# Kernel optimization log

Hardware: AMD Instinct MI355X
Metric: run time of the kernel (lower is better)

## Reference

```python
import jax, jax.numpy as jnp
import numpy as np

NUM_TREES = 150
ARITY = 4
DEPTH = 4
NUM_LEVELS = DEPTH + 1  # leaves (level 0) ... root (level DEPTH)
VOCAB = 10000
SUBTOK = 8
EMB_DIM = 256
HID = 256
NUM_CLASSES = 2


def _build_forest():
    # perfect ARITY-ary tree, level-order indexing; edges point child -> parent
    n = (ARITY ** (DEPTH + 1) - 1) // (ARITY - 1)  # 341
    src = np.arange(1, n)
    dst = (src - 1) // ARITY
    depth_of = np.zeros(n, dtype=np.int64)
    for j in range(1, n):
        depth_of[j] = depth_of[(j - 1) // ARITY] + 1
    level_of = DEPTH - depth_of  # leaves = 0, processed first (topo order)
    offs = np.arange(NUM_TREES) * n
    edge_src = (src[None, :] + offs[:, None]).ravel().astype(np.int32)
    edge_dst = (dst[None, :] + offs[:, None]).ravel().astype(np.int32)
    node_level = np.tile(level_of, NUM_TREES).astype(np.int32)
    graph_id = np.repeat(np.arange(NUM_TREES), n).astype(np.int32)
    leaf_mask = (node_level == 0).astype(np.int32)
    return edge_src, edge_dst, node_level, graph_id, leaf_mask, NUM_TREES * n


def setup_inputs() -> dict:
    key = jax.random.key(0)
    ks = jax.random.split(key, 16)
    es, ed, lvl, gid, lm, N = _build_forest()
    s_e = 1.0 / np.sqrt(EMB_DIM)
    s_h = 1.0 / np.sqrt(HID)
    s_f = 1.0 / np.sqrt(2 * HID)
    return {
        "node_feat1": jax.random.randint(ks[0], (N, SUBTOK), 0, VOCAB, dtype=jnp.int32),
        "node_feat2": jax.random.randint(ks[1], (N, SUBTOK), 0, VOCAB, dtype=jnp.int32),
        "emb1": jax.random.normal(ks[2], (VOCAB, EMB_DIM), jnp.float32) * 0.02,
        "emb2": jax.random.normal(ks[3], (VOCAB, EMB_DIM), jnp.float32) * 0.02,
        "W_iou1": jax.random.normal(ks[4], (EMB_DIM, 3 * HID), jnp.float32) * s_e,
        "W_iou2": jax.random.normal(ks[5], (EMB_DIM, 3 * HID), jnp.float32) * s_e,
        "U_iou1": jax.random.normal(ks[6], (HID, 3 * HID), jnp.float32) * s_h,
        "U_iou2": jax.random.normal(ks[7], (HID, 3 * HID), jnp.float32) * s_h,
        "Uf_W1": jax.random.normal(ks[8], (HID, HID), jnp.float32) * s_h,
        "Uf_b1": jnp.zeros((HID,), jnp.float32),
        "Uf_W2": jax.random.normal(ks[9], (HID, HID), jnp.float32) * s_h,
        "Uf_b2": jnp.zeros((HID,), jnp.float32),
        "b_iou1": jnp.zeros((3 * HID,), jnp.float32),
        "b_iou2": jnp.zeros((3 * HID,), jnp.float32),
        "Wf": jax.random.normal(ks[10], (2 * HID, NUM_CLASSES), jnp.float32) * s_f,
        "bf": jnp.zeros((NUM_CLASSES,), jnp.float32),
        "edge_src": jnp.asarray(es),
        "edge_dst": jnp.asarray(ed),
        "node_level": jnp.asarray(lvl),
        "graph_id": jnp.asarray(gid),
        "leaf_mask": jnp.asarray(lm),
    }


def _tree_lstm(iou0, U_iou, Uf_W, Uf_b, b_iou, edge_src, edge_dst, node_level):
    # ChildSum TreeLSTM, propagated level-by-level (leaves -> root)
    N = iou0.shape[0]
    h = jnp.zeros((N, HID), iou0.dtype)
    c = jnp.zeros((N, HID), iou0.dtype)
    for lvl in range(NUM_LEVELS):
        emask = (node_level[edge_dst] == lvl).astype(h.dtype)[:, None]  # [E,1]
        hs = h[edge_src] * emask  # children h (already computed at lower levels)
        f = jax.nn.sigmoid(hs @ Uf_W + Uf_b)  # per-edge forget gate
        h_tild = jax.ops.segment_sum(hs, edge_dst, num_segments=N)
        c_sum = jax.ops.segment_sum(f * c[edge_src] * emask, edge_dst, num_segments=N)
        has_child = jax.ops.segment_sum(emask, edge_dst, num_segments=N) > 0  # [N,1]
        # DGL semantics: reduce overwrites iou for internal nodes; leaves keep W_iou(x)*mask
        iou = jnp.where(has_child, h_tild @ U_iou, iou0) + b_iou
        i, o, u = jnp.split(iou, 3, axis=1)
        c_new = jax.nn.sigmoid(i) * jnp.tanh(u) + c_sum
        h_new = jax.nn.sigmoid(o) * jnp.tanh(c_new)
        at = (node_level == lvl)[:, None]
        h = jnp.where(at, h_new, h)
        c = jnp.where(at, c_new, c)
    return h


def _branch(node_feat, emb, W_iou, U_iou, Uf_W, Uf_b, b_iou,
            leaf_mask, edge_src, edge_dst, node_level, graph_id):
    embeds = emb[node_feat].mean(axis=1)  # subtoken mean pooling -> [N, EMB_DIM]
    iou0 = (embeds @ W_iou) * leaf_mask.astype(embeds.dtype)[:, None]
    h = _tree_lstm(iou0, U_iou, Uf_W, Uf_b, b_iou, edge_src, edge_dst, node_level)
    s = jax.ops.segment_sum(h, graph_id, num_segments=NUM_TREES)
    cnt = jax.ops.segment_sum(jnp.ones((h.shape[0],), h.dtype), graph_id, num_segments=NUM_TREES)
    return jax.nn.relu(s / cnt[:, None])  # mean graph readout + relu


def reference(node_feat1, node_feat2, emb1, emb2, W_iou1, W_iou2, U_iou1, U_iou2,
              Uf_W1, Uf_b1, Uf_W2, Uf_b2, b_iou1, b_iou2, Wf, bf,
              edge_src, edge_dst, node_level, graph_id, leaf_mask):
    m1 = _branch(node_feat1, emb1, W_iou1, U_iou1, Uf_W1, Uf_b1, b_iou1,
                 leaf_mask, edge_src, edge_dst, node_level, graph_id)
    m2 = _branch(node_feat2, emb2, W_iou2, U_iou2, Uf_W2, Uf_b2, b_iou2,
                 leaf_mask, edge_src, edge_dst, node_level, graph_id)
    logits = jax.nn.leaky_relu(jnp.concatenate([m1, m2], axis=1) @ Wf + bf, 0.01)
    return jax.nn.softmax(logits, axis=-1)
```

## Files before the change

### kernel.cpp

```cpp
#include <hip/hip_runtime.h>

#define NT 150
#define NPT 341
#define LEAF0 85
#define NL (NT*256)
#define NN (NT*NPT)
#define VOCAB 10000

typedef __attribute__((ext_vector_type(8))) short short8;
typedef __attribute__((ext_vector_type(4))) float floatx4;

__device__ __forceinline__ float sigf(float x){ return 1.0f/(1.0f+__expf(-x)); }
__device__ __forceinline__ float bf2f(ushort u){ union{unsigned i; float f;} v; v.i = ((unsigned)u)<<16; return v.f; }
__device__ __forceinline__ ushort f2bf(float x){ union{float f; unsigned i;} v; v.f = x; return (ushort)((v.i + 0x7fff + ((v.i>>16)&1))>>16); }

__global__ __launch_bounds__(256) void convW_k(
    const float* __restrict__ W1, const float* __restrict__ U1, const float* __restrict__ F1,
    const float* __restrict__ W2, const float* __restrict__ U2, const float* __restrict__ F2,
    ushort* Wt1, ushort* Ut1, ushort* Ft1, ushort* Wt2, ushort* Ut2, ushort* Ft2){
  __shared__ float T[32][33];
  const float* src; ushort* dst; int N;
  switch (blockIdx.z){
    case 0: src=W1; dst=Wt1; N=768; break;
    case 1: src=U1; dst=Ut1; N=768; break;
    case 2: src=F1; dst=Ft1; N=256; break;
    case 3: src=W2; dst=Wt2; N=768; break;
    case 4: src=U2; dst=Ut2; N=768; break;
    default: src=F2; dst=Ft2; N=256; break;
  }
  int n0 = blockIdx.x*32; if (n0 >= N) return;
  int k0 = blockIdx.y*32;
  int nl = threadIdx.x & 31, kb = threadIdx.x >> 5;
  #pragma unroll
  for (int i=0;i<4;i++){ int kk = kb*4+i; T[kk][nl] = src[(size_t)(k0+kk)*N + n0 + nl]; }
  __syncthreads();
  #pragma unroll
  for (int i=0;i<4;i++){ int nn = kb*4+i; dst[(size_t)(n0+nn)*256 + k0 + nl] = f2bf(T[nl][nn]); }
}

__global__ __launch_bounds__(256) void convE_k(
    const float* __restrict__ e1, const float* __restrict__ e2,
    ushort* __restrict__ E1, ushort* __restrict__ E2){
  const float* s = blockIdx.y ? e2 : e1;
  ushort* d = blockIdx.y ? E2 : E1;
  size_t i = ((size_t)blockIdx.x*256 + threadIdx.x)*4;
  float4 v = *(const float4*)&s[i];
  d[i+0]=f2bf(v.x); d[i+1]=f2bf(v.y); d[i+2]=f2bf(v.z); d[i+3]=f2bf(v.w);
}

__global__ __launch_bounds__(1024) void leaf_k(
    const int* __restrict__ f1, const int* __restrict__ f2,
    const ushort* __restrict__ E1, const ushort* __restrict__ E2,
    const ushort* __restrict__ Wt1, const float* __restrict__ b1,
    const ushort* __restrict__ Wt2, const float* __restrict__ b2,
    ushort* __restrict__ h1, ushort* __restrict__ c1,
    ushort* __restrict__ h2, ushort* __restrict__ c2){
  __shared__ __attribute__((aligned(16))) ushort As[8][64*40];
  int br = blockIdx.y;
  const int* feat = br ? f2 : f1;
  const ushort* E = br ? E2 : E1;
  const ushort* Wt = br ? Wt2 : Wt1;
  const float* biou = br ? b2 : b1;
  ushort* h = br ? h2 : h1;
  ushort* c = br ? c2 : c1;
  int tid = threadIdx.x;
  int lane = tid & 63, wav = tid >> 6, quad = lane >> 4, l15 = lane & 15;
  int rowbase = blockIdx.x*64;

  {
    int row = tid >> 4, seg = tid & 15;
    int leaf = rowbase + row;
    int tree = leaf >> 8;
    size_t node = (size_t)tree*NPT + LEAF0 + (leaf & 255);
    const int* f = feat + node*8;
    float s[16];
    #pragma unroll
    for (int q=0;q<16;q++) s[q]=0.f;
    #pragma unroll
    for (int j=0;j<8;j++){
      const ushort* rp = E + (size_t)f[j]*256 + seg*16;
      short8 a = *(const short8*)rp;
      short8 b = *(const short8*)(rp+8);
      #pragma unroll
      for (int q=0;q<8;q++){ s[q]+=bf2f((ushort)a[q]); s[8+q]+=bf2f((ushort)b[q]); }
    }
    short8 o1, o2;
    #pragma unroll
    for (int q=0;q<8;q++){ o1[q]=(short)f2bf(s[q]*0.125f); o2[q]=(short)f2bf(s[8+q]*0.125f); }
    int cch = seg >> 1, off = (seg & 1)*16;
    *(short8*)&As[cch][row*40 + off]     = o1;
    *(short8*)&As[cch][row*40 + off + 8] = o2;
  }
  __syncthreads();

  floatx4 acc[3][4];
  #pragma unroll
  for (int g=0;g<3;g++)
    #pragma unroll
    for (int r=0;r<4;r++) acc[g][r] = (floatx4){0.f,0.f,0.f,0.f};

  const ushort* bp0 = Wt + (size_t)(0*256 + wav*16 + l15)*256 + quad*8;
  const ushort* bp1 = Wt + (size_t)(1*256 + wav*16 + l15)*256 + quad*8;
  const ushort* bp2 = Wt + (size_t)(2*256 + wav*16 + l15)*256 + quad*8;

  #pragma unroll
  for (int cch=0; cch<8; cch++){
    short8 b0 = *(const short8*)(bp0 + cch*32);
    short8 b1 = *(const short8*)(bp1 + cch*32);
    short8 b2 = *(const short8*)(bp2 + cch*32);
    #pragma unroll
    for (int r=0;r<4;r++){
      short8 a = *(const short8*)&As[cch][(16*r + l15)*40 + quad*8];
      acc[0][r] = __builtin_amdgcn_mfma_f32_16x16x32_bf16(a, b0, acc[0][r], 0,0,0);
      acc[1][r] = __builtin_amdgcn_mfma_f32_16x16x32_bf16(a, b1, acc[1][r], 0,0,0);
      acc[2][r] = __builtin_amdgcn_mfma_f32_16x16x32_bf16(a, b2, acc[2][r], 0,0,0);
    }
  }
  int hc = wav*16 + l15;
  float bi = biou[hc], bo = biou[256+hc], bu = biou[512+hc];
  #pragma unroll
  for (int r=0;r<4;r++){
    #pragma unroll
    for (int reg=0;reg<4;reg++){
      int leaf = rowbase + 16*r + quad*4 + reg;
      int tree = leaf >> 8;
      size_t node = (size_t)tree*NPT + LEAF0 + (leaf & 255);
      float iv = acc[0][r][reg] + bi;
      float ov = acc[1][r][reg] + bo;
      float uv = acc[2][r][reg] + bu;
      float cc = sigf(iv)*tanhf(uv);
      float hh = sigf(ov)*tanhf(cc);
      h[node*256 + hc] = f2bf(hh);
      c[node*256 + hc] = f2bf(cc);
    }
  }
}

__global__ __launch_bounds__(256) void level_k(
    const ushort* __restrict__ Ut1, const ushort* __restrict__ Ft1,
    const float* __restrict__ Ufb1, const float* __restrict__ bi1,
    const ushort* __restrict__ Ut2, const ushort* __restrict__ Ft2,
    const float* __restrict__ Ufb2, const float* __restrict__ bi2,
    ushort* __restrict__ h1, ushort* __restrict__ c1,
    ushort* __restrict__ h2, ushort* __restrict__ c2,
    int M, int shift, int base, int ncb){
  __shared__ __attribute__((aligned(16))) ushort Ch[8][64*40];
  int br = blockIdx.z;
  const ushort* Ut = br ? Ut2 : Ut1;
  const ushort* Ft = br ? Ft2 : Ft1;
  const float* Ufb = br ? Ufb2 : Ufb1;
  const float* biou = br ? bi2 : bi1;
  ushort* h = br ? h2 : h1;
  ushort* c = br ? c2 : c1;
  int tid = threadIdx.x;
  int lane = tid & 63, wav = tid >> 6, quad = lane >> 4, l15 = lane & 15;
  int m0 = blockIdx.x*16;
  int cb0 = blockIdx.y*ncb;
  int mask = (1<<shift)-1;

  {
    int cl = tid >> 2, q4 = tid & 3;
    int sm = m0 + (cl >> 2); if (sm > M-1) sm = M-1;
    int stree = sm >> shift, sloc = base + (sm & mask);
    const ushort* sgp = h + ((size_t)stree*NPT + 4*sloc + 1 + (cl & 3))*256 + q4*8;
    #pragma unroll
    for (int cc=0;cc<8;cc++)
      *(short8*)&Ch[cc][cl*40 + q4*8] = *(const short8*)(sgp + cc*32);
  }
  __syncthreads();

  for (int p=0; p<ncb; p++){
    int col = (cb0+p)*64 + wav*16 + l15;
    const ushort* bfp = Ft + (size_t)col*256 + quad*8;
    const ushort* bp0 = Ut + (size_t)(0*256 + col)*256 + quad*8;
    const ushort* bp1 = Ut + (size_t)(256 + col)*256 + quad*8;
    const ushort* bp2 = Ut + (size_t)(512 + col)*256 + quad*8;

    floatx4 af[4], ai[4], ao[4], au[4];
    #pragma unroll
    for (int r=0;r<4;r++){
      af[r] = (floatx4){0.f,0.f,0.f,0.f}; ai[r] = (floatx4){0.f,0.f,0.f,0.f};
      ao[r] = (floatx4){0.f,0.f,0.f,0.f}; au[r] = (floatx4){0.f,0.f,0.f,0.f};
    }

    #pragma unroll
    for (int cc=0; cc<8; cc++){
      short8 Bf = *(const short8*)(bfp + cc*32);
      short8 Bi = *(const short8*)(bp0 + cc*32);
      short8 Bo = *(const short8*)(bp1 + cc*32);
      short8 Bu = *(const short8*)(bp2 + cc*32);
      #pragma unroll
      for (int r=0;r<4;r++){
        short8 a = *(const short8*)&Ch[cc][(16*r + l15)*40 + quad*8];
        af[r] = __builtin_amdgcn_mfma_f32_16x16x32_bf16(a, Bf, af[r], 0,0,0);
        ai[r] = __builtin_amdgcn_mfma_f32_16x16x32_bf16(a, Bi, ai[r], 0,0,0);
        ao[r] = __builtin_amdgcn_mfma_f32_16x16x32_bf16(a, Bo, ao[r], 0,0,0);
        au[r] = __builtin_amdgcn_mfma_f32_16x16x32_bf16(a, Bu, au[r], 0,0,0);
      }
    }

    float ufb = Ufb[col];
    float bI = biou[col], bO = biou[256+col], bU = biou[512+col];
    #pragma unroll
    for (int r=0;r<4;r++){
      int m = m0 + 4*r + quad;
      int mm = m < M ? m : M-1;
      int tree = mm >> shift, loc = base + (mm & mask);
      size_t ch0 = ((size_t)tree*NPT + 4*loc + 1)*256 + col;
      float cs = 0.f;
      #pragma unroll
      for (int reg=0;reg<4;reg++)
        cs += sigf(af[r][reg] + ufb) * bf2f(c[ch0 + (size_t)reg*256]);
      float iv = ai[r][0]+ai[r][1]+ai[r][2]+ai[r][3] + bI;
      float ov = ao[r][0]+ao[r][1]+ao[r][2]+ao[r][3] + bO;
      float uv = au[r][0]+au[r][1]+au[r][2]+au[r][3] + bU;
      float cn = sigf(iv)*tanhf(uv) + cs;
      float hn = sigf(ov)*tanhf(cn);
      if (m < M){
        size_t off = ((size_t)tree*NPT + loc)*256 + col;
        h[off] = f2bf(hn);
        c[off] = f2bf(cn);
      }
    }
  }
}

__global__ __launch_bounds__(256) void readout_k(
    const ushort* __restrict__ h1, const ushort* __restrict__ h2,
    float* __restrict__ mp1, float* __restrict__ mp2){
  int br = blockIdx.z, part = blockIdx.y, tree = blockIdx.x;
  const ushort* h = br ? h2 : h1;
  float* mp = br ? mp2 : mp1;
  int t = threadIdx.x;
  int start = part*85;
  int cnt = (part==3) ? 86 : 85;
  const ushort* hp = h + ((size_t)tree*NPT + start)*256 + t;
  float s0=0.f,s1=0.f,s2=0.f,s3=0.f;
  int i = 0;
  for (; i+4<=cnt; i+=4){
    s0 += bf2f(hp[(size_t)(i+0)*256]); s1 += bf2f(hp[(size_t)(i+1)*256]);
    s2 += bf2f(hp[(size_t)(i+2)*256]); s3 += bf2f(hp[(size_t)(i+3)*256]);
  }
  for (; i<cnt; i++) s0 += bf2f(hp[(size_t)i*256]);
  mp[((size_t)tree*4 + part)*256 + t] = s0+s1+s2+s3;
}

__global__ __launch_bounds__(64) void final_k(const float* __restrict__ mp1,
    const float* __restrict__ mp2, const float* __restrict__ Wf,
    const float* __restrict__ bf, float* __restrict__ out){
  int tree = blockIdx.x; int t = threadIdx.x;
  float p0=0.f, p1=0.f;
  for (int k=t;k<512;k+=64){
    const float* mp = (k<256) ? mp1 : mp2;
    int kk = k & 255;
    size_t b0 = ((size_t)tree*4)*256 + kk;
    float s = mp[b0] + mp[b0+256] + mp[b0+512] + mp[b0+768];
    float x = fmaxf(s*(1.0f/341.0f), 0.f);
    p0 += x*Wf[k*2+0]; p1 += x*Wf[k*2+1];
  }
  #pragma unroll
  for (int off=32; off>0; off>>=1){
    p0 += __shfl_down(p0, off);
    p1 += __shfl_down(p1, off);
  }
  if (t==0){
    float l0 = p0+bf[0], l1 = p1+bf[1];
    l0 = (l0>0.f)?l0:0.01f*l0;
    l1 = (l1>0.f)?l1:0.01f*l1;
    float mx = fmaxf(l0,l1);
    float e0 = __expf(l0-mx), e1 = __expf(l1-mx);
    float inv = 1.0f/(e0+e1);
    out[tree*2+0] = e0*inv; out[tree*2+1] = e1*inv;
  }
}

extern "C" void kernel_launch(void* const* d_in, const int* in_sizes, int n_in,
                              void* d_out, int out_size, void* d_ws, size_t ws_size,
                              hipStream_t stream) {
  const int*   feat1 = (const int*)  d_in[0];
  const int*   feat2 = (const int*)  d_in[1];
  const float* emb1  = (const float*)d_in[2];
  const float* emb2  = (const float*)d_in[3];
  const float* Wiou1 = (const float*)d_in[4];
  const float* Wiou2 = (const float*)d_in[5];
  const float* Uiou1 = (const float*)d_in[6];
  const float* Uiou2 = (const float*)d_in[7];
  const float* UfW1  = (const float*)d_in[8];
  const float* Ufb1  = (const float*)d_in[9];
  const float* UfW2  = (const float*)d_in[10];
  const float* Ufb2  = (const float*)d_in[11];
  const float* biou1 = (const float*)d_in[12];
  const float* biou2 = (const float*)d_in[13];
  const float* Wf    = (const float*)d_in[14];
  const float* bfv   = (const float*)d_in[15];
  float* out = (float*)d_out;

  char* ws = (char*)d_ws;
  ushort* h1  = (ushort*)ws;  ws += (size_t)NN*256*2;
  ushort* h2  = (ushort*)ws;  ws += (size_t)NN*256*2;
  ushort* c1  = (ushort*)ws;  ws += (size_t)NN*256*2;
  ushort* c2  = (ushort*)ws;  ws += (size_t)NN*256*2;
  ushort* E1  = (ushort*)ws;  ws += (size_t)VOCAB*256*2;
  ushort* E2  = (ushort*)ws;  ws += (size_t)VOCAB*256*2;
  ushort* Wt1 = (ushort*)ws;  ws += 768*256*2;
  ushort* Ut1 = (ushort*)ws;  ws += 768*256*2;
  ushort* Ft1 = (ushort*)ws;  ws += 256*256*2;
  ushort* Wt2 = (ushort*)ws;  ws += 768*256*2;
  ushort* Ut2 = (ushort*)ws;  ws += 768*256*2;
  ushort* Ft2 = (ushort*)ws;  ws += 256*256*2;
  float*  mp1 = (float*)ws;   ws += (size_t)NT*4*256*4;
  float*  mp2 = (float*)ws;   ws += (size_t)NT*4*256*4;

  convE_k<<<dim3(2500, 2), 256, 0, stream>>>(emb1, emb2, E1, E2);
  convW_k<<<dim3(24, 8, 6), 256, 0, stream>>>(Wiou1, Uiou1, UfW1, Wiou2, Uiou2, UfW2,
                                              Wt1, Ut1, Ft1, Wt2, Ut2, Ft2);
  leaf_k<<<dim3(NL/64, 2), 1024, 0, stream>>>(feat1, feat2, E1, E2,
                                              Wt1, biou1, Wt2, biou2, h1, c1, h2, c2);

  const int lvlM[4]     = {9600, 2400, 600, 150};
  const int lvlShift[4] = {6, 4, 2, 0};
  const int lvlBase[4]  = {21, 5, 1, 0};
  const int lvlGy[4]    = {1, 1, 2, 4};
  const int lvlNcb[4]   = {4, 4, 2, 1};
  for (int l=0;l<4;l++){
    int gx = (lvlM[l] + 15)/16;
    level_k<<<dim3(gx, lvlGy[l], 2), 256, 0, stream>>>(Ut1, Ft1, Ufb1, biou1,
                                                       Ut2, Ft2, Ufb2, biou2,
                                                       h1, c1, h2, c2,
                                                       lvlM[l], lvlShift[l], lvlBase[l], lvlNcb[l]);
  }
  readout_k<<<dim3(NT, 4, 2), 256, 0, stream>>>(h1, h2, mp1, mp2);
  final_k<<<NT, 64, 0, stream>>>(mp1, mp2, Wf, bfv, out);
}
```

Baseline: 445.8 us.

## Split level kernel across column blocks and read children directly without LDS staging

The level kernel now always launches four column blocks per row tile, each handling 64 output columns, instead of looping over several column blocks inside one workgroup. Child hidden states are read straight from global memory into MFMA operands rather than staged through shared memory with a barrier. Child cell states are prefetched into registers before the matrix loop. This raises parallelism on the larger levels and removes LDS traffic and synchronisation. In exchange, each block rereads the child h rows from global/L2, with some redundancy across column blocks.

```diff
diff --git a/kernel.cpp b/kernel.cpp
--- a/kernel.cpp
+++ b/kernel.cpp
@@ -143,8 +143,7 @@
     const float* __restrict__ Ufb2, const float* __restrict__ bi2,
     ushort* __restrict__ h1, ushort* __restrict__ c1,
     ushort* __restrict__ h2, ushort* __restrict__ c2,
-    int M, int shift, int base, int ncb){
-  __shared__ __attribute__((aligned(16))) ushort Ch[8][64*40];
+    int M, int shift, int base){
   int br = blockIdx.z;
   const ushort* Ut = br ? Ut2 : Ut1;
   const ushort* Ft = br ? Ft2 : Ft1;
@@ -154,73 +153,77 @@
   ushort* c = br ? c2 : c1;
   int tid = threadIdx.x;
   int lane = tid & 63, wav = tid >> 6, quad = lane >> 4, l15 = lane & 15;
-  int m0 = blockIdx.x*16;
-  int cb0 = blockIdx.y*ncb;
+  int m0 = blockIdx.x*16, cb = blockIdx.y;
   int mask = (1<<shift)-1;
-
-  {
-    int cl = tid >> 2, q4 = tid & 3;
-    int sm = m0 + (cl >> 2); if (sm > M-1) sm = M-1;
-    int stree = sm >> shift, sloc = base + (sm & mask);
-    const ushort* sgp = h + ((size_t)stree*NPT + 4*sloc + 1 + (cl & 3))*256 + q4*8;
-    #pragma unroll
-    for (int cc=0;cc<8;cc++)
-      *(short8*)&Ch[cc][cl*40 + q4*8] = *(const short8*)(sgp + cc*32);
-  }
-  __syncthreads();
-
-  for (int p=0; p<ncb; p++){
-    int col = (cb0+p)*64 + wav*16 + l15;
-    const ushort* bfp = Ft + (size_t)col*256 + quad*8;
-    const ushort* bp0 = Ut + (size_t)(0*256 + col)*256 + quad*8;
-    const ushort* bp1 = Ut + (size_t)(256 + col)*256 + quad*8;
-    const ushort* bp2 = Ut + (size_t)(512 + col)*256 + quad*8;
-
-    floatx4 af[4], ai[4], ao[4], au[4];
+  int col = cb*64 + wav*16 + l15;
+
+  const ushort* arow[4];
+  #pragma unroll
+  for (int r=0;r<4;r++){
+    int row = 16*r + l15;
+    int m = m0 + (row>>2); if (m > M-1) m = M-1;
+    int tree = m >> shift, loc = base + (m & mask);
+    arow[r] = h + ((size_t)tree*NPT + 4*loc + 1 + (row&3))*256 + quad*8;
+  }
+
+  float cv[4][4];
+  #pragma unroll
+  for (int r=0;r<4;r++){
+    int m = m0 + 4*r + quad; int mm = m < M ? m : M-1;
+    int tree = mm >> shift, loc = base + (mm & mask);
+    const ushort* cp = c + ((size_t)tree*NPT + 4*loc + 1)*256 + col;
+    #pragma unroll
+    for (int reg=0;reg<4;reg++) cv[r][reg] = bf2f(cp[(size_t)reg*256]);
+  }
+
+  const ushort* bfp = Ft + (size_t)col*256 + quad*8;
+  const ushort* bp0 = Ut + (size_t)(0*256 + col)*256 + quad*8;
+  const ushort* bp1 = Ut + (size_t)(256 + col)*256 + quad*8;
+  const ushort* bp2 = Ut + (size_t)(512 + col)*256 + quad*8;
+
+  floatx4 af[4], ai[4], ao[4], au[4];
+  #pragma unroll
+  for (int r=0;r<4;r++){
+    af[r] = (floatx4){0.f,0.f,0.f,0.f}; ai[r] = (floatx4){0.f,0.f,0.f,0.f};
+    ao[r] = (floatx4){0.f,0.f,0.f,0.f}; au[r] = (floatx4){0.f,0.f,0.f,0.f};
+  }
+
+  #pragma unroll
+  for (int cc=0; cc<8; cc++){
+    short8 Bf = *(const short8*)(bfp + cc*32);
+    short8 Bi = *(const short8*)(bp0 + cc*32);
+    short8 Bo = *(const short8*)(bp1 + cc*32);
+    short8 Bu = *(const short8*)(bp2 + cc*32);
     #pragma unroll
     for (int r=0;r<4;r++){
-      af[r] = (floatx4){0.f,0.f,0.f,0.f}; ai[r] = (floatx4){0.f,0.f,0.f,0.f};
-      ao[r] = (floatx4){0.f,0.f,0.f,0.f}; au[r] = (floatx4){0.f,0.f,0.f,0.f};
-    }
-
-    #pragma unroll
-    for (int cc=0; cc<8; cc++){
-      short8 Bf = *(const short8*)(bfp + cc*32);
-      short8 Bi = *(const short8*)(bp0 + cc*32);
-      short8 Bo = *(const short8*)(bp1 + cc*32);
-      short8 Bu = *(const short8*)(bp2 + cc*32);
-      #pragma unroll
-      for (int r=0;r<4;r++){
-        short8 a = *(const short8*)&Ch[cc][(16*r + l15)*40 + quad*8];
-        af[r] = __builtin_amdgcn_mfma_f32_16x16x32_bf16(a, Bf, af[r], 0,0,0);
-        ai[r] = __builtin_amdgcn_mfma_f32_16x16x32_bf16(a, Bi, ai[r], 0,0,0);
-        ao[r] = __builtin_amdgcn_mfma_f32_16x16x32_bf16(a, Bo, ao[r], 0,0,0);
-        au[r] = __builtin_amdgcn_mfma_f32_16x16x32_bf16(a, Bu, au[r], 0,0,0);
-      }
-    }
-
-    float ufb = Ufb[col];
-    float bI = biou[col], bO = biou[256+col], bU = biou[512+col];
-    #pragma unroll
-    for (int r=0;r<4;r++){
-      int m = m0 + 4*r + quad;
-      int mm = m < M ? m : M-1;
-      int tree = mm >> shift, loc = base + (mm & mask);
-      size_t ch0 = ((size_t)tree*NPT + 4*loc + 1)*256 + col;
-      float cs = 0.f;
-      #pragma unroll
-      for (int reg=0;reg<4;reg++)
-        cs += sigf(af[r][reg] + ufb) * bf2f(c[ch0 + (size_t)reg*256]);
-      float iv = ai[r][0]+ai[r][1]+ai[r][2]+ai[r][3] + bI;
-      float ov = ao[r][0]+ao[r][1]+ao[r][2]+ao[r][3] + bO;
-      float uv = au[r][0]+au[r][1]+au[r][2]+au[r][3] + bU;
-      float cn = sigf(iv)*tanhf(uv) + cs;
-      float hn = sigf(ov)*tanhf(cn);
-      if (m < M){
-        size_t off = ((size_t)tree*NPT + loc)*256 + col;
-        h[off] = f2bf(hn);
-        c[off] = f2bf(cn);
-      }
+      short8 a = *(const short8*)(arow[r] + cc*32);
+      af[r] = __builtin_amdgcn_mfma_f32_16x16x32_bf16(a, Bf, af[r], 0,0,0);
+      ai[r] = __builtin_amdgcn_mfma_f32_16x16x32_bf16(a, Bi, ai[r], 0,0,0);
+      ao[r] = __builtin_amdgcn_mfma_f32_16x16x32_bf16(a, Bo, ao[r], 0,0,0);
+      au[r] = __builtin_amdgcn_mfma_f32_16x16x32_bf16(a, Bu, au[r], 0,0,0);
+    }
+  }
+
+  float ufb = Ufb[col];
+  float bI = biou[col], bO = biou[256+col], bU = biou[512+col];
+  #pragma unroll
+  for (int r=0;r<4;r++){
+    int m = m0 + 4*r + quad;
+    int mm = m < M ? m : M-1;
+    int tree = mm >> shift, loc = base + (mm & mask);
+    float cs = 0.f;
+    #pragma unroll
+    for (int reg=0;reg<4;reg++)
+      cs += sigf(af[r][reg] + ufb) * cv[r][reg];
+    float iv = ai[r][0]+ai[r][1]+ai[r][2]+ai[r][3] + bI;
+    float ov = ao[r][0]+ao[r][1]+ao[r][2]+ao[r][3] + bO;
+    float uv = au[r][0]+au[r][1]+au[r][2]+au[r][3] + bU;
+    float cn = sigf(iv)*tanhf(uv) + cs;
+    float hn = sigf(ov)*tanhf(cn);
+    if (m < M){
+      size_t off = ((size_t)tree*NPT + loc)*256 + col;
+      h[off] = f2bf(hn);
+      c[off] = f2bf(cn);
     }
   }
 }
@@ -320,14 +323,12 @@
   const int lvlM[4]     = {9600, 2400, 600, 150};
   const int lvlShift[4] = {6, 4, 2, 0};
   const int lvlBase[4]  = {21, 5, 1, 0};
-  const int lvlGy[4]    = {1, 1, 2, 4};
-  const int lvlNcb[4]   = {4, 4, 2, 1};
   for (int l=0;l<4;l++){
     int gx = (lvlM[l] + 15)/16;
-    level_k<<<dim3(gx, lvlGy[l], 2), 256, 0, stream>>>(Ut1, Ft1, Ufb1, biou1,
-                                                       Ut2, Ft2, Ufb2, biou2,
-                                                       h1, c1, h2, c2,
-                                                       lvlM[l], lvlShift[l], lvlBase[l], lvlNcb[l]);
+    level_k<<<dim3(gx, 4, 2), 256, 0, stream>>>(Ut1, Ft1, Ufb1, biou1,
+                                                Ut2, Ft2, Ufb2, biou2,
+                                                h1, c1, h2, c2,
+                                                lvlM[l], lvlShift[l], lvlBase[l]);
   }
   readout_k<<<dim3(NT, 4, 2), 256, 0, stream>>>(h1, h2, mp1, mp2);
   final_k<<<NT, 64, 0, stream>>>(mp1, mp2, Wf, bfv, out);
```

After: 454.8 us. 1.02x slower.
